# Performance work log

Measured on AMD Instinct MI355X. Metric: run time of the kernel, lower is better.

The kernel has to match this reference:

```python
import jax, jax.numpy as jnp
import numpy as np


def setup_inputs() -> dict:
    key = jax.random.key(0)
    k1, k2 = jax.random.split(key)
    B, D = 1048576, 16
    model_out = jax.random.normal(k1, (B, D), dtype=jnp.float32)
    y_true = jax.random.normal(k2, (B, D), dtype=jnp.float32)
    return {"model_out": model_out, "y_true": y_true}


def _elem_loss(x, y):
    # nn.MSELoss(reduction='none'): elementwise squared error
    return (x - y) ** 2


def reference(model_out, y_true):
    # loss: [B, D] elementwise
    loss = _elem_loss(model_out, y_true)

    # d_loss = d(loss.sum())/d(model_out), same shape as model_out
    d_loss = jax.grad(lambda x: _elem_loss(x, y_true).sum())(model_out)

    # sqd_loss[b, i, j] = d^2 loss / d x[b,i] d x[b,j].
    # Loss is elementwise (no cross-batch coupling), so the Hessian is
    # block-diagonal over batch: compute a [D, D] per-sample Hessian via
    # vmap(jacfwd(grad)) instead of the torch per-dim autograd loop.
    def per_sample_grad(x_b, y_b):  # [D] -> [D]
        return jax.grad(lambda x: _elem_loss(x, y_b).sum())(x_b)

    sqd_loss = jax.vmap(
        lambda x_b, y_b: jax.jacfwd(per_sample_grad)(x_b, y_b)
    )(model_out, y_true)  # [B, D, D]

    return loss, d_loss, sqd_loss
```

## Files before the change

### kernel.cpp

```cpp
#include <hip/hip_runtime.h>


__global__ __launch_bounds__(256) void loss_grad_kernel(
    const float4* __restrict__ x,
    const float4* __restrict__ y,
    float4* __restrict__ loss,
    float4* __restrict__ dloss,
    int n4) {
    int i = blockIdx.x * blockDim.x + threadIdx.x;
    if (i >= n4) return;
    float4 a = x[i];
    float4 b = y[i];
    float4 d;
    d.x = a.x - b.x;
    d.y = a.y - b.y;
    d.z = a.z - b.z;
    d.w = a.w - b.w;
    float4 l;
    l.x = d.x * d.x;
    l.y = d.y * d.y;
    l.z = d.z * d.z;
    l.w = d.w * d.w;
    float4 g;
    g.x = 2.0f * d.x;
    g.y = 2.0f * d.y;
    g.z = 2.0f * d.z;
    g.w = 2.0f * d.w;
    loss[i] = l;
    dloss[i] = g;
}

__global__ __launch_bounds__(256) void hess_fill_kernel(
    float4* __restrict__ out, unsigned int n4) {
    unsigned int i = blockIdx.x * blockDim.x + threadIdx.x;
    if (i >= n4) return;
    unsigned int f = i << 2;
    unsigned int col = f & 15u;
    unsigned int row = (f >> 4) & 15u;
    float4 v;
    v.x = (row == col)      ? 2.0f : 0.0f;
    v.y = (row == col + 1u) ? 2.0f : 0.0f;
    v.z = (row == col + 2u) ? 2.0f : 0.0f;
    v.w = (row == col + 3u) ? 2.0f : 0.0f;
    out[i] = v;
}

extern "C" void kernel_launch(void* const* d_in, const int* in_sizes, int n_in,
                              void* d_out, int out_size, void* d_ws, size_t ws_size,
                              hipStream_t stream) {
    const float* model_out = (const float*)d_in[0];
    const float* y_true    = (const float*)d_in[1];
    float* out = (float*)d_out;

    const int BD = in_sizes[0];
    float* loss_p  = out;
    float* dloss_p = out + BD;
    float* sqd_p   = out + 2 * (size_t)BD;

    {
        int n4 = BD / 4;
        int block = 256;
        int grid = (n4 + block - 1) / block;
        loss_grad_kernel<<<grid, block, 0, stream>>>(
            (const float4*)model_out, (const float4*)y_true,
            (float4*)loss_p, (float4*)dloss_p, n4);
    }

    {
        unsigned int n4 = (unsigned int)((size_t)BD * 16 / 4);
        int block = 256;
        unsigned int grid = (n4 + block - 1) / block;
        hess_fill_kernel<<<grid, block, 0, stream>>>((float4*)sqd_p, n4);
    }
}
```

Measured before the change: 1.234 ms.

## Fuse loss/grad and Hessian fill into one grid-stride kernel with nontemporal stores

Merges the two launches into a single persistent grid-stride kernel with a fixed grid of 2048 blocks. The loss and gradient are written first, then the constant diagonal Hessian pattern is written. The Hessian vector is computed once per thread, which works because the grid stride is a multiple of 64 vectors, so each thread always lands on the same position in the pattern. All stores use nontemporal hints to avoid polluting the cache on this write-bound workload. The aim is to save one launch and cut per-thread index arithmetic, at the risk that a fixed grid underutilizes bandwidth.

```diff
diff --git a/kernel.cpp b/kernel.cpp
--- a/kernel.cpp
+++ b/kernel.cpp
@@ -1,48 +1,43 @@
 #include <hip/hip_runtime.h>
 
 
-__global__ __launch_bounds__(256) void loss_grad_kernel(
-    const float4* __restrict__ x,
-    const float4* __restrict__ y,
-    float4* __restrict__ loss,
-    float4* __restrict__ dloss,
-    int n4) {
-    int i = blockIdx.x * blockDim.x + threadIdx.x;
-    if (i >= n4) return;
-    float4 a = x[i];
-    float4 b = y[i];
-    float4 d;
-    d.x = a.x - b.x;
-    d.y = a.y - b.y;
-    d.z = a.z - b.z;
-    d.w = a.w - b.w;
-    float4 l;
-    l.x = d.x * d.x;
-    l.y = d.y * d.y;
-    l.z = d.z * d.z;
-    l.w = d.w * d.w;
-    float4 g;
-    g.x = 2.0f * d.x;
-    g.y = 2.0f * d.y;
-    g.z = 2.0f * d.z;
-    g.w = 2.0f * d.w;
-    loss[i] = l;
-    dloss[i] = g;
-}
+typedef float v4f __attribute__((ext_vector_type(4)));
 
-__global__ __launch_bounds__(256) void hess_fill_kernel(
-    float4* __restrict__ out, unsigned int n4) {
-    unsigned int i = blockIdx.x * blockDim.x + threadIdx.x;
-    if (i >= n4) return;
-    unsigned int f = i << 2;
-    unsigned int col = f & 15u;
-    unsigned int row = (f >> 4) & 15u;
-    float4 v;
-    v.x = (row == col)      ? 2.0f : 0.0f;
-    v.y = (row == col + 1u) ? 2.0f : 0.0f;
-    v.z = (row == col + 2u) ? 2.0f : 0.0f;
-    v.w = (row == col + 3u) ? 2.0f : 0.0f;
-    out[i] = v;
+__global__ __launch_bounds__(256) void fused_loss_hess(
+    const v4f* __restrict__ x,
+    const v4f* __restrict__ y,
+    v4f* __restrict__ loss,
+    v4f* __restrict__ dloss,
+    v4f* __restrict__ sqd,
+    unsigned int n4_ld,
+    unsigned int n4_h) {
+    const unsigned int T   = gridDim.x * blockDim.x;
+    const unsigned int tid = blockIdx.x * blockDim.x + threadIdx.x;
+
+    for (unsigned int i = tid; i < n4_ld; i += T) {
+        v4f a = x[i];
+        v4f b = y[i];
+        v4f d = a - b;
+        v4f l = d * d;
+        v4f g = d + d;
+        __builtin_nontemporal_store(l, &loss[i]);
+        __builtin_nontemporal_store(g, &dloss[i]);
+    }
+
+    {
+        const unsigned int f   = tid << 2;
+        const unsigned int col = f & 15u;
+        const unsigned int row = (f >> 4) & 15u;
+        v4f v;
+        v.x = (row == col)      ? 2.0f : 0.0f;
+        v.y = (row == col + 1u) ? 2.0f : 0.0f;
+        v.z = (row == col + 2u) ? 2.0f : 0.0f;
+        v.w = (row == col + 3u) ? 2.0f : 0.0f;
+#pragma unroll 8
+        for (unsigned int i = tid; i < n4_h; i += T) {
+            __builtin_nontemporal_store(v, &sqd[i]);
+        }
+    }
 }
 
 extern "C" void kernel_launch(void* const* d_in, const int* in_sizes, int n_in,
@@ -57,19 +52,13 @@
     float* dloss_p = out + BD;
     float* sqd_p   = out + 2 * (size_t)BD;
 
-    {
-        int n4 = BD / 4;
-        int block = 256;
-        int grid = (n4 + block - 1) / block;
-        loss_grad_kernel<<<grid, block, 0, stream>>>(
-            (const float4*)model_out, (const float4*)y_true,
-            (float4*)loss_p, (float4*)dloss_p, n4);
-    }
+    const unsigned int n4_ld = (unsigned int)(BD / 4);
+    const unsigned int n4_h  = (unsigned int)((size_t)BD * 16 / 4);
 
-    {
-        unsigned int n4 = (unsigned int)((size_t)BD * 16 / 4);
-        int block = 256;
-        unsigned int grid = (n4 + block - 1) / block;
-        hess_fill_kernel<<<grid, block, 0, stream>>>((float4*)sqd_p, n4);
-    }
+    const int block = 256;
+    const int grid  = 2048;
+    fused_loss_hess<<<grid, block, 0, stream>>>(
+        (const v4f*)model_out, (const v4f*)y_true,
+        (v4f*)loss_p, (v4f*)dloss_p, (v4f*)sqd_p,
+        n4_ld, n4_h);
 }
```

Result: slower. 1.296 ms (+5.0%).
